# Optimization experiments

Hardware: AMD Instinct MI355X
Metric: run time of the kernel (lower is better)

## Reference

```python
import jax, jax.numpy as jnp
import numpy as np

DIM, HEADS, HEAD_DIM = 1024, 16, 64
B, S = 2, 1024
LAMBDA = 4.0
EPS = 1e-6


def setup_inputs() -> dict:
    key = jax.random.key(0)
    ks = jax.random.split(key, 7)
    sc = 1.0 / np.sqrt(DIM)
    return {
        "x": jax.random.normal(ks[0], (B, S, DIM), jnp.float32),
        "qkv_w": jax.random.normal(ks[1], (3 * DIM, DIM), jnp.float32) * sc,
        "qkv_b": jax.random.normal(ks[2], (3 * DIM,), jnp.float32) * 0.01,
        "proj_w": jax.random.normal(ks[3], (DIM, DIM), jnp.float32) * sc,
        "proj_b": jax.random.normal(ks[4], (DIM,), jnp.float32) * 0.01,
        "dwc_w": jax.random.normal(ks[5], (DIM, 1, 3), jnp.float32) * 0.3,
        "dwc_b": jax.random.normal(ks[6], (DIM,), jnp.float32) * 0.01,
    }


def _l1_dist(q, k):
    # q,k: [B,H,S,Dh] -> pairwise L1 distance [B,H,S,S].
    # Accumulate over head_dim with a (rematerialized) scan so we never
    # materialize the [B,H,S,S,Dh] broadcast tensor.
    qT = jnp.moveaxis(q, -1, 0)  # [Dh,B,H,S]
    kT = jnp.moveaxis(k, -1, 0)

    def step(acc, qk):
        qd, kd = qk  # [B,H,S]
        return acc + jnp.abs(qd[..., :, None] - kd[..., None, :]), None

    init = jnp.zeros(q.shape[:-1] + (k.shape[-2],), q.dtype)
    dist, _ = jax.lax.scan(jax.checkpoint(step), init, (qT, kT))
    return dist


def reference(x, qkv_w, qkv_b, proj_w, proj_b, dwc_w, dwc_b):
    Bq, Sq, C = x.shape
    # qkv projection -> q,k,v each [B,H,S,Dh]
    qkv = (x @ qkv_w.T + qkv_b).reshape(Bq, Sq, 3, HEADS, HEAD_DIM)
    qkv = jnp.transpose(qkv, (2, 0, 3, 1, 4))
    q, k, v = qkv[0], qkv[1], qkv[2]

    # exact Laplacian (L1-distance) kernel attention, row-normalized
    dist = _l1_dist(q, k)                       # [B,H,S,S]
    kern = jnp.exp(-LAMBDA * dist / HEAD_DIM)   # mean-L1 scaling
    attn = kern / (jnp.sum(kern, axis=-1, keepdims=True) + EPS)
    global_attn = jnp.einsum("bhij,bhjd->bhid", attn, v)

    # depthwise conv1d local branch on v (channel order = head-major)
    v1d = jnp.transpose(v, (0, 1, 3, 2)).reshape(Bq, C, Sq)  # [B,C,S]
    local = jax.lax.conv_general_dilated(
        v1d, dwc_w, window_strides=(1,), padding=((1, 1),),
        feature_group_count=C, dimension_numbers=("NCH", "OIH", "NCH"))
    local = local + dwc_b[None, :, None]
    local = jnp.transpose(local.reshape(Bq, HEADS, HEAD_DIM, Sq), (0, 1, 3, 2))

    y = global_attn + local                      # [B,H,S,Dh]
    y = jnp.transpose(y, (0, 2, 1, 3)).reshape(Bq, Sq, C)
    return y @ proj_w.T + proj_b
```

## Files before the change

kernel.cpp:

```cpp
#include <hip/hip_runtime.h>

#define DIMC 1024
#define HEADS 16
#define HD 64
#define BATCH 2
#define SEQ 1024
#define NQKV 3072

typedef _Float16 f16;
typedef _Float16 half8 __attribute__((ext_vector_type(8)));
typedef _Float16 half4v __attribute__((ext_vector_type(4)));
typedef float floatx4 __attribute__((ext_vector_type(4)));

__device__ __forceinline__ void gld16(const void* g, void* l) {
  __builtin_amdgcn_global_load_lds((const __attribute__((address_space(1))) void*)g,
                                   (__attribute__((address_space(3))) void*)l, 16, 0, 0);
}

__device__ __forceinline__ unsigned sadU8(unsigned a, unsigned b, unsigned c) {
#if __has_builtin(__builtin_amdgcn_sad_u8)
  return __builtin_amdgcn_sad_u8(a, b, c);
#else
  unsigned d;
  asm("v_sad_u8 %0, %1, %2, %3" : "=v"(d) : "v"(a), "v"(b), "v"(c));
  return d;
#endif
}

__global__ __launch_bounds__(256) void cvt_kernel(
    const float* __restrict__ x, const float* __restrict__ wq, const float* __restrict__ wp,
    f16* __restrict__ x16, f16* __restrict__ wq16, f16* __restrict__ wp16)
{
  int bid = blockIdx.x;
  const float* src; f16* dst; int base;
  if (bid < 512)        { src = x;  dst = x16;  base = bid; }
  else if (bid < 1280)  { src = wq; dst = wq16; base = bid - 512; }
  else                  { src = wp; dst = wp16; base = bid - 1280; }
  long long i0 = (long long)base*1024 + threadIdx.x;
#pragma unroll
  for (int k2 = 0; k2 < 4; ++k2) {
    long long i = i0 + k2*256;
    float4 v = ((const float4*)src)[i];
    half4v h; h[0]=(f16)v.x; h[1]=(f16)v.y; h[2]=(f16)v.z; h[3]=(f16)v.w;
    *(half4v*)(dst + i*4) = h;
  }
}

template<int TM, int TN, int BK, int MW, int MODE>
__global__ __launch_bounds__(256, MW) void gemm_kernel(
    const f16* __restrict__ A, const f16* __restrict__ Bw, const float* __restrict__ bias,
    unsigned char* __restrict__ q8, unsigned char* __restrict__ k8, f16* __restrict__ vT,
    float* __restrict__ outp, int K)
{
  constexpr int MT = TM / 32;
  constexpr int NT = TN / 32;
  constexpr int G  = BK / 8;
  __shared__ f16 As[TM*BK];
  __shared__ f16 Bs[TN*BK];
  const int tid = threadIdx.x;
  const int wave = tid >> 6, lane = tid & 63;
  const int lq = lane >> 4, li = lane & 15;
  const int m0 = blockIdx.y * TM, n0 = blockIdx.x * TN;
  const int wm = (wave & 1) * (TM/2), wn = (wave >> 1) * (TN/2);
  floatx4 acc[MT][NT] = {};

  const int kIters = K / BK;
  for (int kt = 0; kt < kIters; ++kt) {
    __syncthreads();
#pragma unroll
    for (int r = 0; r < TM*BK/2048; ++r) {
      int slot = r*256 + tid;
      int row = slot / G, c = slot % G, g = c ^ (row & (G-1));
      gld16(A + (size_t)(m0+row)*K + kt*BK + g*8, As + slot*8);
    }
#pragma unroll
    for (int r = 0; r < TN*BK/2048; ++r) {
      int slot = r*256 + tid;
      int row = slot / G, c = slot % G, g = c ^ (row & (G-1));
      gld16(Bw + (size_t)(n0+row)*K + kt*BK + g*8, Bs + slot*8);
    }
    __syncthreads();
#pragma unroll
    for (int ks = 0; ks < BK/32; ++ks) {
      half8 af[MT], bf[NT];
      int kc = ks*4 + lq;
#pragma unroll
      for (int t = 0; t < MT; ++t) {
        int am = wm + t*16 + li;
        af[t] = *(const half8*)&As[am*BK + (kc ^ (am & (G-1)))*8];
      }
#pragma unroll
      for (int t = 0; t < NT; ++t) {
        int bn = wn + t*16 + li;
        bf[t] = *(const half8*)&Bs[bn*BK + (kc ^ (bn & (G-1)))*8];
      }
#pragma unroll
      for (int mt = 0; mt < MT; ++mt)
#pragma unroll
        for (int nt = 0; nt < NT; ++nt)
          acc[mt][nt] = __builtin_amdgcn_mfma_f32_16x16x32_f16(af[mt], bf[nt], acc[mt][nt], 0, 0, 0);
    }
  }

#pragma unroll
  for (int mt = 0; mt < MT; ++mt) {
#pragma unroll
    for (int nt = 0; nt < NT; ++nt) {
      int f = n0 + wn + nt*16 + li;
      float bb = bias[f];
      if (MODE == 0) {
        int which = f >> 10, cc = f & 1023, h = cc >> 6, d = cc & 63;
        int t0 = m0 + wm + mt*16 + lq*4;
        int b = t0 >> 10, s0 = t0 & 1023;
        if (which == 2) {
          half4v hv;
#pragma unroll
          for (int r = 0; r < 4; ++r) hv[r] = (f16)(acc[mt][nt][r] + bb);
          *(half4v*)&vT[((size_t)((b*HEADS + h)*HD + d))*SEQ + s0] = hv;
        } else {
          unsigned char* dst = (which == 0) ? q8 : k8;
#pragma unroll
          for (int r = 0; r < 4; ++r) {
            float v = acc[mt][nt][r] + bb;
            int u = (int)floorf(v * 16.0f + 128.5f);
            u = u < 0 ? 0 : (u > 255 ? 255 : u);
            dst[((size_t)((b*HEADS + h)*SEQ + s0 + r))*HD + d] = (unsigned char)u;
          }
        }
      } else {
#pragma unroll
        for (int r = 0; r < 4; ++r) {
          int t = m0 + wm + mt*16 + lq*4 + r;
          outp[(size_t)t*DIMC + f] = acc[mt][nt][r] + bb;
        }
      }
    }
  }
}

__global__ __launch_bounds__(256, 3) void attn_kernel(
    const unsigned char* __restrict__ q8g, const unsigned char* __restrict__ k8g,
    const f16* __restrict__ vTg, const float* __restrict__ dwcw, const float* __restrict__ dwcb,
    f16* __restrict__ y16)
{
  __shared__ unsigned char q8s[64*64];
  __shared__ unsigned char k8s[128*64];
  __shared__ f16 vTs[64*128];
  __shared__ f16 sfrag[16*64*8];
  __shared__ float rowsum[64];
  __shared__ f16 vconv[64*66];

  const int tid = threadIdx.x;
  const int bh = blockIdx.y;
  const int i0 = blockIdx.x * 64;
  const int lane = tid & 63, wave = tid >> 6;
  const int lq = lane >> 4, li = lane & 15;
  const int iL = tid & 15, jt = tid >> 4;
  const int ksj = jt >> 2, qj = jt & 3;

  if (tid < 64) rowsum[tid] = 1e-6f;

  {
    gld16(q8g + ((size_t)(bh*SEQ) + i0)*HD + tid*16, q8s + tid*16);
  }
  {
    int d = tid >> 2, part = tid & 3;
    const f16* vrow = vTg + ((size_t)(bh*HD) + d)*SEQ;
#pragma unroll
    for (int e = 0; e < 17; ++e) {
      int ss = part*17 + e;
      if (ss < 66) {
        int s = i0 - 1 + ss;
        vconv[d*66 + ss] = (s >= 0 && s < SEQ) ? vrow[s] : (f16)0.0f;
      }
    }
  }
  __syncthreads();

  unsigned qr[4][16];
#pragma unroll
  for (int n = 0; n < 4; ++n)
#pragma unroll
    for (int c4 = 0; c4 < 4; ++c4) {
      uint4 t = *(const uint4*)&q8s[(iL + n*16)*64 + c4*16];
      qr[n][c4*4+0] = t.x; qr[n][c4*4+1] = t.y; qr[n][c4*4+2] = t.z; qr[n][c4*4+3] = t.w;
    }

  float rs[4] = {0.f, 0.f, 0.f, 0.f};
  floatx4 pacc[2][2] = {};
  const int mtb = (wave & 1) * 2, ntb = (wave >> 1) * 2;

  for (int jb = 0; jb < 8; ++jb) {
    const int j0 = jb * 128;
    __syncthreads();
#pragma unroll
    for (int r = 0; r < 2; ++r) {
      int slot = r*256 + tid;
      gld16(k8g + ((size_t)(bh*SEQ) + j0)*HD + slot*16, k8s + slot*16);
    }
#pragma unroll
    for (int r = 0; r < 4; ++r) {
      int slot = r*256 + tid;
      int d = slot >> 4, c = slot & 15, sc = c ^ (d & 7);
      gld16(vTg + ((size_t)(bh*HD) + d)*SEQ + j0 + sc*8, vTs + slot*8);
    }
    __syncthreads();

    unsigned sacc[4][8] = {};
#pragma unroll
    for (int c4 = 0; c4 < 4; ++c4) {
      uint4 kk[8];
#pragma unroll
      for (int jj = 0; jj < 8; ++jj)
        kk[jj] = *(const uint4*)&k8s[(jt*8 + jj)*64 + c4*16];
#pragma unroll
      for (int n = 0; n < 4; ++n)
#pragma unroll
        for (int jj = 0; jj < 8; ++jj) {
          sacc[n][jj] = sadU8(qr[n][c4*4+0], kk[jj].x, sacc[n][jj]);
          sacc[n][jj] = sadU8(qr[n][c4*4+1], kk[jj].y, sacc[n][jj]);
          sacc[n][jj] = sadU8(qr[n][c4*4+2], kk[jj].z, sacc[n][jj]);
          sacc[n][jj] = sadU8(qr[n][c4*4+3], kk[jj].w, sacc[n][jj]);
        }
    }
#pragma unroll
    for (int n = 0; n < 4; ++n) {
      half8 sv;
#pragma unroll
      for (int jj = 0; jj < 8; ++jj) {
        float sf = exp2f(-0.0056355275f * (float)sacc[n][jj]);
        rs[n] += sf;
        sv[jj] = (f16)sf;
      }
      *(half8*)&sfrag[((n*4 + ksj)*64 + qj*16 + iL)*8] = sv;
    }
    __syncthreads();

#pragma unroll
    for (int ks = 0; ks < 4; ++ks) {
      half8 a0 = *(const half8*)&sfrag[(((mtb+0)*4 + ks)*64 + lane)*8];
      half8 a1 = *(const half8*)&sfrag[(((mtb+1)*4 + ks)*64 + lane)*8];
#pragma unroll
      for (int nt = 0; nt < 2; ++nt) {
        int d = (ntb + nt)*16 + li;
        int kc = ks*4 + lq;
        half8 bfr = *(const half8*)&vTs[d*128 + (kc ^ (d & 7))*8];
        pacc[0][nt] = __builtin_amdgcn_mfma_f32_16x16x32_f16(a0, bfr, pacc[0][nt], 0, 0, 0);
        pacc[1][nt] = __builtin_amdgcn_mfma_f32_16x16x32_f16(a1, bfr, pacc[1][nt], 0, 0, 0);
      }
    }
  }

#pragma unroll
  for (int n = 0; n < 4; ++n) {
    rs[n] += __shfl_xor(rs[n], 16, 64);
    rs[n] += __shfl_xor(rs[n], 32, 64);
  }
  if (lane < 16) {
#pragma unroll
    for (int n = 0; n < 4; ++n) atomicAdd(&rowsum[lane + n*16], rs[n]);
  }
  __syncthreads();

  const int b = bh >> 4, h = bh & 15;
#pragma unroll
  for (int nt = 0; nt < 2; ++nt) {
    int d = (ntb + nt)*16 + li;
    int c = h*64 + d;
    float w0 = dwcw[c*3+0], w1 = dwcw[c*3+1], w2 = dwcw[c*3+2], cb = dwcb[c];
#pragma unroll
    for (int mt = 0; mt < 2; ++mt)
#pragma unroll
      for (int r = 0; r < 4; ++r) {
        int ii = (mtb + mt)*16 + lq*4 + r;
        float val = pacc[mt][nt][r] / rowsum[ii];
        val += w0*(float)vconv[d*66 + ii] + w1*(float)vconv[d*66 + ii + 1]
             + w2*(float)vconv[d*66 + ii + 2] + cb;
        int s = i0 + ii;
        y16[((size_t)(b*SEQ + s))*DIMC + c] = (f16)val;
      }
  }
}

extern "C" void kernel_launch(void* const* d_in, const int* in_sizes, int n_in,
                              void* d_out, int out_size, void* d_ws, size_t ws_size,
                              hipStream_t stream) {
  const float* x      = (const float*)d_in[0];
  const float* qkv_w  = (const float*)d_in[1];
  const float* qkv_b  = (const float*)d_in[2];
  const float* proj_w = (const float*)d_in[3];
  const float* proj_b = (const float*)d_in[4];
  const float* dwc_w  = (const float*)d_in[5];
  const float* dwc_b  = (const float*)d_in[6];
  float* out = (float*)d_out;

  char* ws = (char*)d_ws;
  f16* x16  = (f16*)(ws);
  f16* wq16 = (f16*)(ws + (4ll<<20));
  f16* wp16 = (f16*)(ws + (10ll<<20));
  unsigned char* q8 = (unsigned char*)(ws + (12ll<<20));
  unsigned char* k8 = (unsigned char*)(ws + (14ll<<20));
  f16* vT   = (f16*)(ws + (16ll<<20));
  f16* y16  = (f16*)(ws + (20ll<<20));

  cvt_kernel<<<1536, 256, 0, stream>>>(x, qkv_w, proj_w, x16, wq16, wp16);
  gemm_kernel<128,128,128,2,0><<<dim3(24, 16), 256, 0, stream>>>(x16, wq16, qkv_b, q8, k8, vT, nullptr, DIMC);
  attn_kernel<<<dim3(16, 32), 256, 0, stream>>>(q8, k8, vT, dwc_w, dwc_b, y16);
  gemm_kernel<64,64,128,4,1><<<dim3(16, 32), 256, 0, stream>>>(y16, wp16, proj_b, nullptr, nullptr, nullptr, out, DIMC);
}
```

Before: 154.9 us.

## Halve attention query tile to 32 rows and swizzle K shared-memory layout

Each attention block now handles 32 query rows instead of 64, which doubles the grid to 1024 blocks. The SAD score work per thread is cut to 4 keys, and the thread-to-row mapping, sfrag layout, MFMA wave assignment and rowsum reduction are remapped to match. K rows are XOR-swizzled in LDS to reduce bank conflicts on the 16-byte reads. The goal is better CU occupancy and load balance on the 256-CU part, at the cost of loading K and V tiles twice as often across the grid.

```diff
diff --git a/kernel.cpp b/kernel.cpp
--- a/kernel.cpp
+++ b/kernel.cpp
@@ -143,35 +143,35 @@
     const f16* __restrict__ vTg, const float* __restrict__ dwcw, const float* __restrict__ dwcb,
     f16* __restrict__ y16)
 {
-  __shared__ unsigned char q8s[64*64];
+  __shared__ unsigned char q8s[32*64];
   __shared__ unsigned char k8s[128*64];
   __shared__ f16 vTs[64*128];
-  __shared__ f16 sfrag[16*64*8];
-  __shared__ float rowsum[64];
-  __shared__ f16 vconv[64*66];
+  __shared__ f16 sfrag[8*64*8];
+  __shared__ float rowsum[32];
+  __shared__ f16 vconv[64*34];
 
   const int tid = threadIdx.x;
   const int bh = blockIdx.y;
-  const int i0 = blockIdx.x * 64;
+  const int i0 = blockIdx.x * 32;
   const int lane = tid & 63, wave = tid >> 6;
   const int lq = lane >> 4, li = lane & 15;
-  const int iL = tid & 15, jt = tid >> 4;
-  const int ksj = jt >> 2, qj = jt & 3;
-
-  if (tid < 64) rowsum[tid] = 1e-6f;
-
-  {
+  const int iL = tid & 7, jt = tid >> 3;
+  const int mtw = wave & 1, dh = wave >> 1;
+
+  if (tid < 32) rowsum[tid] = 1e-6f;
+
+  if (wave < 2)
     gld16(q8g + ((size_t)(bh*SEQ) + i0)*HD + tid*16, q8s + tid*16);
-  }
+
   {
     int d = tid >> 2, part = tid & 3;
     const f16* vrow = vTg + ((size_t)(bh*HD) + d)*SEQ;
 #pragma unroll
-    for (int e = 0; e < 17; ++e) {
-      int ss = part*17 + e;
-      if (ss < 66) {
+    for (int e = 0; e < 9; ++e) {
+      int ss = part*9 + e;
+      if (ss < 34) {
         int s = i0 - 1 + ss;
-        vconv[d*66 + ss] = (s >= 0 && s < SEQ) ? vrow[s] : (f16)0.0f;
+        vconv[d*34 + ss] = (s >= 0 && s < SEQ) ? vrow[s] : (f16)0.0f;
       }
     }
   }
@@ -182,13 +182,12 @@
   for (int n = 0; n < 4; ++n)
 #pragma unroll
     for (int c4 = 0; c4 < 4; ++c4) {
-      uint4 t = *(const uint4*)&q8s[(iL + n*16)*64 + c4*16];
+      uint4 t = *(const uint4*)&q8s[(iL + 8*n)*64 + c4*16];
       qr[n][c4*4+0] = t.x; qr[n][c4*4+1] = t.y; qr[n][c4*4+2] = t.z; qr[n][c4*4+3] = t.w;
     }
 
   float rs[4] = {0.f, 0.f, 0.f, 0.f};
-  floatx4 pacc[2][2] = {};
-  const int mtb = (wave & 1) * 2, ntb = (wave >> 1) * 2;
+  floatx4 pacc[2] = {};
 
   for (int jb = 0; jb < 8; ++jb) {
     const int j0 = jb * 128;
@@ -196,7 +195,8 @@
 #pragma unroll
     for (int r = 0; r < 2; ++r) {
       int slot = r*256 + tid;
-      gld16(k8g + ((size_t)(bh*SEQ) + j0)*HD + slot*16, k8s + slot*16);
+      int row = slot >> 2, c = slot & 3, g = c ^ ((row >> 2) & 3);
+      gld16(k8g + ((size_t)(bh*SEQ) + j0)*HD + row*64 + g*16, k8s + slot*16);
     }
 #pragma unroll
     for (int r = 0; r < 4; ++r) {
@@ -206,17 +206,17 @@
     }
     __syncthreads();
 
-    unsigned sacc[4][8] = {};
+    unsigned sacc[4][4] = {};
 #pragma unroll
     for (int c4 = 0; c4 < 4; ++c4) {
-      uint4 kk[8];
-#pragma unroll
-      for (int jj = 0; jj < 8; ++jj)
-        kk[jj] = *(const uint4*)&k8s[(jt*8 + jj)*64 + c4*16];
+      uint4 kk[4];
+#pragma unroll
+      for (int jj = 0; jj < 4; ++jj)
+        kk[jj] = *(const uint4*)&k8s[(jt*4 + jj)*64 + ((c4 ^ (jt & 3))*16)];
 #pragma unroll
       for (int n = 0; n < 4; ++n)
 #pragma unroll
-        for (int jj = 0; jj < 8; ++jj) {
+        for (int jj = 0; jj < 4; ++jj) {
           sacc[n][jj] = sadU8(qr[n][c4*4+0], kk[jj].x, sacc[n][jj]);
           sacc[n][jj] = sadU8(qr[n][c4*4+1], kk[jj].y, sacc[n][jj]);
           sacc[n][jj] = sadU8(qr[n][c4*4+2], kk[jj].z, sacc[n][jj]);
@@ -225,60 +225,58 @@
     }
 #pragma unroll
     for (int n = 0; n < 4; ++n) {
-      half8 sv;
-#pragma unroll
-      for (int jj = 0; jj < 8; ++jj) {
+      half4v sv;
+#pragma unroll
+      for (int jj = 0; jj < 4; ++jj) {
         float sf = exp2f(-0.0056355275f * (float)sacc[n][jj]);
         rs[n] += sf;
         sv[jj] = (f16)sf;
       }
-      *(half8*)&sfrag[((n*4 + ksj)*64 + qj*16 + iL)*8] = sv;
+      *(half4v*)&sfrag[(((n>>1)*4 + (jt>>3))*64 + iL + 8*(n&1) + 16*((jt>>1)&3))*8
+                       + (jt&1)*4] = sv;
     }
     __syncthreads();
 
 #pragma unroll
     for (int ks = 0; ks < 4; ++ks) {
-      half8 a0 = *(const half8*)&sfrag[(((mtb+0)*4 + ks)*64 + lane)*8];
-      half8 a1 = *(const half8*)&sfrag[(((mtb+1)*4 + ks)*64 + lane)*8];
+      half8 a = *(const half8*)&sfrag[((mtw*4 + ks)*64 + lane)*8];
 #pragma unroll
       for (int nt = 0; nt < 2; ++nt) {
-        int d = (ntb + nt)*16 + li;
+        int d = dh*32 + nt*16 + li;
         int kc = ks*4 + lq;
         half8 bfr = *(const half8*)&vTs[d*128 + (kc ^ (d & 7))*8];
-        pacc[0][nt] = __builtin_amdgcn_mfma_f32_16x16x32_f16(a0, bfr, pacc[0][nt], 0, 0, 0);
-        pacc[1][nt] = __builtin_amdgcn_mfma_f32_16x16x32_f16(a1, bfr, pacc[1][nt], 0, 0, 0);
+        pacc[nt] = __builtin_amdgcn_mfma_f32_16x16x32_f16(a, bfr, pacc[nt], 0, 0, 0);
       }
     }
   }
 
 #pragma unroll
   for (int n = 0; n < 4; ++n) {
+    rs[n] += __shfl_xor(rs[n], 8, 64);
     rs[n] += __shfl_xor(rs[n], 16, 64);
     rs[n] += __shfl_xor(rs[n], 32, 64);
   }
-  if (lane < 16) {
-#pragma unroll
-    for (int n = 0; n < 4; ++n) atomicAdd(&rowsum[lane + n*16], rs[n]);
+  if (lane < 8) {
+#pragma unroll
+    for (int n = 0; n < 4; ++n) atomicAdd(&rowsum[lane + 8*n], rs[n]);
   }
   __syncthreads();
 
   const int b = bh >> 4, h = bh & 15;
 #pragma unroll
   for (int nt = 0; nt < 2; ++nt) {
-    int d = (ntb + nt)*16 + li;
+    int d = dh*32 + nt*16 + li;
     int c = h*64 + d;
     float w0 = dwcw[c*3+0], w1 = dwcw[c*3+1], w2 = dwcw[c*3+2], cb = dwcb[c];
 #pragma unroll
-    for (int mt = 0; mt < 2; ++mt)
-#pragma unroll
-      for (int r = 0; r < 4; ++r) {
-        int ii = (mtb + mt)*16 + lq*4 + r;
-        float val = pacc[mt][nt][r] / rowsum[ii];
-        val += w0*(float)vconv[d*66 + ii] + w1*(float)vconv[d*66 + ii + 1]
-             + w2*(float)vconv[d*66 + ii + 2] + cb;
-        int s = i0 + ii;
-        y16[((size_t)(b*SEQ + s))*DIMC + c] = (f16)val;
-      }
+    for (int r = 0; r < 4; ++r) {
+      int ii = mtw*16 + lq*4 + r;
+      float val = pacc[nt][r] / rowsum[ii];
+      val += w0*(float)vconv[d*34 + ii] + w1*(float)vconv[d*34 + ii + 1]
+           + w2*(float)vconv[d*34 + ii + 2] + cb;
+      int s = i0 + ii;
+      y16[((size_t)(b*SEQ + s))*DIMC + c] = (f16)val;
+    }
   }
 }
 
@@ -305,6 +303,6 @@
 
   cvt_kernel<<<1536, 256, 0, stream>>>(x, qkv_w, proj_w, x16, wq16, wp16);
   gemm_kernel<128,128,128,2,0><<<dim3(24, 16), 256, 0, stream>>>(x16, wq16, qkv_b, q8, k8, vT, nullptr, DIMC);
-  attn_kernel<<<dim3(16, 32), 256, 0, stream>>>(q8, k8, vT, dwc_w, dwc_b, y16);
+  attn_kernel<<<dim3(32, 32), 256, 0, stream>>>(q8, k8, vT, dwc_w, dwc_b, y16);
   gemm_kernel<64,64,128,4,1><<<dim3(16, 32), 256, 0, stream>>>(y16, wp16, proj_b, nullptr, nullptr, nullptr, out, DIMC);
 }
```

New measurement: 158.0 us. About the same (+2.0%).
